# Performance work log

Hardware: AMD Instinct MI355X
Metric: run time of the kernel (lower is better)

Reference implementation:

```python
import jax, jax.numpy as jnp
import numpy as np

T, A, B_IMG, Z, READ_N, WRITE_N, ENC, DEC, BATCH = 16, 64, 64, 128, 8, 8, 512, 512, 512
EPS = 1e-8


def setup_inputs() -> dict:
    key = jax.random.key(0)
    ks = jax.random.split(key, 16)
    s = 0.05
    n = lambda k, shape: jax.random.normal(k, shape, jnp.float32) * s
    return {
        "x": jax.random.uniform(ks[0], (BATCH, B_IMG * A), jnp.float32),
        "eps": jax.random.normal(ks[1], (T, BATCH, Z), jnp.float32),
        "enc_Wih": n(ks[2], (4 * ENC, 2 * READ_N * READ_N + DEC)),
        "enc_Whh": n(ks[3], (4 * ENC, ENC)),
        "enc_b": jnp.zeros((4 * ENC,), jnp.float32),
        "mu_W": n(ks[4], (Z, ENC)),
        "mu_b": jnp.zeros((Z,), jnp.float32),
        "sig_W": n(ks[5], (Z, ENC)),
        "sig_b": jnp.zeros((Z,), jnp.float32),
        "dec_Wih": n(ks[6], (4 * DEC, Z)),
        "dec_Whh": n(ks[7], (4 * DEC, DEC)),
        "dec_b": jnp.zeros((4 * DEC,), jnp.float32),
        "write_W": n(ks[8], (WRITE_N * WRITE_N, DEC)),
        "write_b": jnp.zeros((WRITE_N * WRITE_N,), jnp.float32),
        "attn_W": n(ks[9], (5, DEC)),
        "attn_b": jnp.zeros((5,), jnp.float32),
    }


def _lstm(x, h, c, Wih, Whh, b):
    g = x @ Wih.T + h @ Whh.T + b  # [bs, 4H]
    i, f, gg, o = jnp.split(g, 4, axis=1)
    c2 = jax.nn.sigmoid(f) * c + jax.nn.sigmoid(i) * jnp.tanh(gg)
    return jax.nn.sigmoid(o) * jnp.tanh(c2), c2


def _filterbank(gx, gy, sigma2, delta, N):
    # gx, gy, sigma2, delta: [bs, 1]
    grid = jnp.arange(N, dtype=jnp.float32)[None, :]  # [1, N]
    mu_x = gx + (grid - 0.5 * N - 0.5) * delta  # [bs, N]
    mu_y = gy + (grid - 0.5 * N - 0.5) * delta
    a = jnp.arange(A, dtype=jnp.float32)
    b = jnp.arange(B_IMG, dtype=jnp.float32)
    s2 = sigma2[:, :, None]  # [bs,1,1]
    Fx = jnp.exp(-((a[None, None, :] - mu_x[:, :, None]) ** 2) / (2 * s2))  # [bs,N,A]
    Fx = Fx / (Fx.sum(2, keepdims=True) + EPS)
    Fy = jnp.exp(-((b[None, None, :] - mu_y[:, :, None]) ** 2) / (2 * s2))  # [bs,N,B]
    Fy = Fy / (Fy.sum(2, keepdims=True) + EPS)
    return Fx, Fy


def _attn_window(h_dec, N, attn_W, attn_b):
    p = h_dec @ attn_W.T + attn_b  # [bs,5]
    gx_, gy_, log_s2, log_d, log_g = jnp.split(p, 5, axis=1)
    gx = (A + 1) * 0.5 * (gx_ + 1)
    gy = (B_IMG + 1) * 0.5 * (gy_ + 1)
    delta = (max(A, B_IMG) - 1) * jnp.exp(log_d) / (N - 1)
    Fx, Fy = _filterbank(gx, gy, jnp.exp(log_s2), delta, N)
    return Fx, Fy, jnp.exp(log_g)  # gamma: [bs,1]


def reference(x, eps, enc_Wih, enc_Whh, enc_b, mu_W, mu_b, sig_W, sig_b,
              dec_Wih, dec_Whh, dec_b, write_W, write_b, attn_W, attn_b):
    bs = x.shape[0]
    img = x.reshape(bs, B_IMG, A)

    def step(carry, e):
        h_enc, c_enc, h_dec, c_dec, canvas = carry
        x_hat = x - jax.nn.sigmoid(canvas)
        # --- read with attention ---
        Fx, Fy, gamma = _attn_window(h_dec, READ_N, attn_W, attn_b)
        def glimpse(im):  # Fy @ im @ Fx^T -> [bs, N, N]
            g = jnp.einsum('bnh,bhw,bmw->bnm', Fy, im, Fx)
            return g.reshape(bs, READ_N * READ_N) * gamma
        r = jnp.concatenate([glimpse(img), glimpse(x_hat.reshape(bs, B_IMG, A))], axis=1)
        # --- encoder LSTM ---
        h_enc, c_enc = _lstm(jnp.concatenate([r, h_dec], 1), h_enc, c_enc, enc_Wih, enc_Whh, enc_b)
        # --- latent sample ---
        mu = h_enc @ mu_W.T + mu_b
        log_sigma = h_enc @ sig_W.T + sig_b
        z = mu + e * jnp.exp(log_sigma)
        # --- decoder LSTM ---
        h_dec, c_dec = _lstm(z, h_dec, c_dec, dec_Wih, dec_Whh, dec_b)
        # --- write with attention ---
        w = (h_dec @ write_W.T + write_b).reshape(bs, WRITE_N, WRITE_N)
        Fx2, Fy2, gamma2 = _attn_window(h_dec, WRITE_N, attn_W, attn_b)
        wr = jnp.einsum('bnh,bnm,bma->bha', Fy2, w, Fx2).reshape(bs, B_IMG * A) / gamma2
        canvas = canvas + wr
        return (h_enc, c_enc, h_dec, c_dec, canvas), canvas

    z32 = jnp.zeros((bs, ENC), jnp.float32)
    init = (z32, z32, jnp.zeros((bs, DEC), jnp.float32), jnp.zeros((bs, DEC), jnp.float32),
            jnp.zeros((bs, B_IMG * A), jnp.float32))
    _, cs = jax.lax.scan(step, init, eps)
    return cs  # [T, bs, B*A]
```

## Files before the change

### kernel.cpp

```cpp
#include <hip/hip_runtime.h>

#define LDF 68
#define EPSF 1e-8f
#define MFMA(A,B,C) __builtin_amdgcn_mfma_f32_16x16x32_bf16((A),(B),(C),0,0,0)

typedef __attribute__((ext_vector_type(8))) short bf16x8;
typedef __attribute__((ext_vector_type(4))) float f32x4;

__device__ __forceinline__ float sigf(float x){ return 1.0f/(1.0f + __expf(-x)); }

__device__ __forceinline__ unsigned short f2bf(float f){
  unsigned u = __float_as_uint(f);
  u += 0x7FFFu + ((u >> 16) & 1u);
  return (unsigned short)(u >> 16);
}
__device__ __forceinline__ float bf2f(unsigned short s){
  return __uint_as_float((unsigned)s << 16);
}

__device__ __forceinline__ size_t pk(int b, int col, int KB){
  return ((((size_t)((b>>4)*KB + (col>>5)))*64) + (size_t)((b&15) + (((col>>3)&3)<<4)))*8 + (col&7);
}

__device__ __forceinline__ void gload_lds16(const void* g, void* l){
  __builtin_amdgcn_global_load_lds(
      (const __attribute__((address_space(1))) void*)g,
      (__attribute__((address_space(3))) void*)l, 16, 0, 0);
}

__global__ void reorder_gates(const float* __restrict__ src, float* __restrict__ dst,
                              int H, int K, int total){
  int idx = blockIdx.x*256 + threadIdx.x;
  if (idx >= total) return;
  int row = idx / K;
  int col = idx - row*K;
  int j = row >> 2, g = row & 3;
  dst[idx] = src[(size_t)(g*H + j)*K + col];
}

__global__ void pack_w_mfma(const float* __restrict__ Wih, const float* __restrict__ Whh,
                            int K_ih, int K_tot,
                            unsigned short* __restrict__ dhi, unsigned short* __restrict__ dlo,
                            int total8){
  int idx = blockIdx.x*256 + threadIdx.x;
  if (idx >= total8) return;
  int lane = idx & 63;
  int rest = idx >> 6;
  int KB = K_tot >> 5;
  int kb = rest % KB;
  int fm = rest / KB;
  int rr = fm*16 + (lane & 15);
  int orow = (rr & 3)*512 + (rr >> 2);
  int k0 = kb*32 + (lane >> 4)*8;
  union { unsigned short s[8]; uint4 u; } vh, vl;
  #pragma unroll
  for (int i = 0; i < 8; i++){
    int k = k0 + i;
    float f = (k < K_ih) ? Wih[(size_t)orow*K_ih + k]
                         : Whh[(size_t)orow*512 + (k - K_ih)];
    unsigned short hi = f2bf(f);
    vh.s[i] = hi;
    vl.s[i] = f2bf(f - bf2f(hi));
  }
  *(uint4*)(dhi + (size_t)idx*8) = vh.u;
  *(uint4*)(dlo + (size_t)idx*8) = vl.u;
}

__global__ void pack_wz_mfma(const float* __restrict__ muW, const float* __restrict__ sigW,
                             unsigned short* __restrict__ dhi, unsigned short* __restrict__ dlo){
  int idx = blockIdx.x*256 + threadIdx.x;
  if (idx >= 16384) return;
  int lane = idx & 63, rest = idx >> 6;
  int kb = rest & 15, fmf = rest >> 4;
  int row = fmf*16 + (lane & 15);
  const float* src = (row < 128) ? (muW + (size_t)row*512) : (sigW + (size_t)(row-128)*512);
  int k0 = kb*32 + (lane >> 4)*8;
  union { unsigned short s[8]; uint4 u; } vh, vl;
  #pragma unroll
  for (int i = 0; i < 8; i++){
    float f = src[k0 + i];
    unsigned short hi = f2bf(f);
    vh.s[i] = hi;
    vl.s[i] = f2bf(f - bf2f(hi));
  }
  *(uint4*)(dhi + (size_t)idx*8) = vh.u;
  *(uint4*)(dlo + (size_t)idx*8) = vl.u;
}

__global__ void transpose_ww(const float* __restrict__ W, float* __restrict__ dst){
  int idx = blockIdx.x*256 + threadIdx.x;
  if (idx >= 512*64) return;
  int k = idx >> 6, n = idx & 63;
  dst[idx] = W[n*512 + k];
}

__global__ void zero_f(float* p, int n){
  int idx = blockIdx.x*256 + threadIdx.x;
  if (idx < n) p[idx] = 0.f;
}

__device__ void attn_window(const float* __restrict__ h,
                            const float* __restrict__ attn_W,
                            const float* __restrict__ attn_b,
                            float* Fx, float* Fy, float* pl)
{
  int tid = threadIdx.x;
  int lane = tid & 63, wid = tid >> 6;
  for (int q = wid; q < 5; q += 4){
    float s = 0.f;
    for (int k = lane; k < 512; k += 64) s += h[k]*attn_W[q*512 + k];
    for (int m = 32; m; m >>= 1) s += __shfl_xor(s, m);
    if (lane == 0) pl[q] = s + attn_b[q];
  }
  __syncthreads();
  float gx    = 32.5f*(pl[0] + 1.f);
  float gy    = 32.5f*(pl[1] + 1.f);
  float s2    = __expf(pl[2]);
  float delta = 9.f*__expf(pl[3]);
  float inv2  = 1.f/(2.f*s2);
  int n = tid >> 5, a = tid & 31;
  float mux = gx + ((float)n - 4.5f)*delta;
  float muy = gy + ((float)n - 4.5f)*delta;
  float dx0 = (float)a      - mux, dx1 = (float)(a+32) - mux;
  float dy0 = (float)a      - muy, dy1 = (float)(a+32) - muy;
  float e0 = __expf(-dx0*dx0*inv2), e1 = __expf(-dx1*dx1*inv2);
  float f0 = __expf(-dy0*dy0*inv2), f1 = __expf(-dy1*dy1*inv2);
  float sx = e0 + e1, sy = f0 + f1;
  for (int m = 16; m; m >>= 1){ sx += __shfl_xor(sx, m); sy += __shfl_xor(sy, m); }
  float rx = 1.f/(sx + EPSF), ry = 1.f/(sy + EPSF);
  Fx[n*LDF + a]      = e0*rx;  Fx[n*LDF + a + 32] = e1*rx;
  Fy[n*LDF + a]      = f0*ry;  Fy[n*LDF + a + 32] = f1*ry;
  __syncthreads();
}

template<int KB>
__global__ __launch_bounds__(512) void mfma_gemm_lstm(
    const bf16x8* __restrict__ Wh, const bf16x8* __restrict__ Wl,
    const unsigned short* __restrict__ act, int actPlane,
    const float4* __restrict__ bias4, const float* __restrict__ c_in,
    float* __restrict__ h_f32, float* __restrict__ c_out,
    unsigned short* __restrict__ out0, int KB0, int off0, int plane0,
    unsigned short* __restrict__ out1, int KB1, int off1, int plane1)
{
  __shared__ __align__(16) unsigned char lds[3][8192];
  const int tid = threadIdx.x, lane = tid & 63, w = tid >> 6;
  const int mt = blockIdx.x & 31, nt = blockIdx.x >> 5;
  const int fm = w & 3, fn0 = (w >> 2) << 1;

  const bf16x8* whp = Wh + ((size_t)(mt*4+fm)*KB)*64 + lane;
  const bf16x8* wlp = Wl + ((size_t)(mt*4+fm)*KB)*64 + lane;

  const char* ast = (const char*)act + (size_t)(w & 1)*((size_t)actPlane*2)
                  + ((size_t)(nt*4 + (w >> 1))*KB)*1024 + (size_t)lane*16;

  const int j0 = (mt*4+fm)*4 + (lane >> 4);
  float4 bb = bias4[j0];
  f32x4 acc0 = {bb.x, bb.y, bb.z, bb.w};
  f32x4 acc1 = acc0;

  gload_lds16(ast, (char*)&lds[0][w*1024]);
  bf16x8 whA = whp[0], wlA = wlp[0];
  __builtin_amdgcn_sched_barrier(0);
  asm volatile("" ::: "memory");
  gload_lds16(ast + 1024, (char*)&lds[1][w*1024]);
  bf16x8 whB = whp[64], wlB = wlp[64];
  __builtin_amdgcn_sched_barrier(0);
  asm volatile("" ::: "memory");

  const size_t rdoff = (size_t)fn0*2048 + (size_t)lane*16;

  #pragma unroll
  for (int kb = 0; kb < KB; kb++){
    asm volatile("s_waitcnt vmcnt(3)" ::: "memory");
    __builtin_amdgcn_s_barrier();
    asm volatile("" ::: "memory");
    __builtin_amdgcn_sched_barrier(0);
    bf16x8 whC = whA, wlC = wlA;
    if (kb + 2 < KB){
      gload_lds16(ast + (size_t)(kb+2)*1024, (char*)&lds[(kb+2)%3][w*1024]);
      whC = whp[(kb+2)*64]; wlC = wlp[(kb+2)*64];
    }
    const unsigned char* rb = &lds[kb%3][0] + rdoff;
    bf16x8 a0h = *(const bf16x8*)(rb);
    bf16x8 a0l = *(const bf16x8*)(rb + 1024);
    bf16x8 a1h = *(const bf16x8*)(rb + 2048);
    bf16x8 a1l = *(const bf16x8*)(rb + 3072);
    acc0 = MFMA(whA, a0h, acc0);
    acc1 = MFMA(whA, a1h, acc1);
    acc0 = MFMA(wlA, a0h, acc0);
    acc1 = MFMA(wlA, a1h, acc1);
    acc0 = MFMA(whA, a0l, acc0);
    acc1 = MFMA(whA, a1l, acc1);
    whA = whB; wlA = wlB; whB = whC; wlB = wlC;
  }

  const int bb0 = nt*64 + fn0*16 + (lane & 15);
  #pragma unroll
  for (int n = 0; n < 2; n++){
    f32x4 g = n ? acc1 : acc0;
    int b = bb0 + n*16;
    float ig = sigf(g[0]);
    float fg = sigf(g[1]);
    float gg = tanhf(g[2]);
    float og = sigf(g[3]);
    float c2 = fg * c_in[(size_t)b*512 + j0] + ig * gg;
    float h  = og * tanhf(c2);
    c_out[(size_t)b*512 + j0] = c2;
    if (h_f32) h_f32[(size_t)b*512 + j0] = h;
    unsigned short hh = f2bf(h);
    unsigned short hl = f2bf(h - bf2f(hh));
    size_t o0 = pk(b, off0 + j0, KB0);
    out0[o0] = hh; out0[o0 + plane0] = hl;
    if (out1){
      size_t o1 = pk(b, off1 + j0, KB1);
      out1[o1] = hh; out1[o1 + plane1] = hl;
    }
  }
}

__global__ __launch_bounds__(64) void zgemm_kernel(
    const bf16x8* __restrict__ Wzh, const bf16x8* __restrict__ Wzl,
    const unsigned short* __restrict__ az, int planeZ,
    const float* __restrict__ mu_b, const float* __restrict__ sig_b,
    const float* __restrict__ eps_t,
    unsigned short* __restrict__ actD, int planeD)
{
  const int fmb = blockIdx.x & 7, cg = blockIdx.x >> 3;
  const int lane = threadIdx.x;
  const bf16x8* wmh = Wzh + (size_t)(fmb    *16)*64 + lane;
  const bf16x8* wml = Wzl + (size_t)(fmb    *16)*64 + lane;
  const bf16x8* wsh = Wzh + (size_t)((fmb+8)*16)*64 + lane;
  const bf16x8* wsl = Wzl + (size_t)((fmb+8)*16)*64 + lane;
  const unsigned short* ab = az + (size_t)cg*8192 + (size_t)lane*8;

  const int r0 = fmb*16 + (lane >> 4)*4;
  float4 bm = *(const float4*)&mu_b[r0];
  float4 bs = *(const float4*)&sig_b[r0];
  f32x4 am = {bm.x, bm.y, bm.z, bm.w};
  f32x4 as = {bs.x, bs.y, bs.z, bs.w};

  #pragma unroll
  for (int kb = 0; kb < 16; kb++){
    bf16x8 ah = *(const bf16x8*)(ab + (size_t)kb*512);
    bf16x8 al = *(const bf16x8*)(ab + planeZ + (size_t)kb*512);
    bf16x8 h0 = wmh[kb*64], l0 = wml[kb*64];
    bf16x8 h1 = wsh[kb*64], l1 = wsl[kb*64];
    am = MFMA(h0, ah, am); am = MFMA(l0, ah, am); am = MFMA(h0, al, am);
    as = MFMA(h1, ah, as); as = MFMA(l1, ah, as); as = MFMA(h1, al, as);
  }

  const int b = cg*16 + (lane & 15);
  float4 ev = *(const float4*)&eps_t[(size_t)b*128 + r0];
  float e[4] = {ev.x, ev.y, ev.z, ev.w};
  union { unsigned short s[4]; uint2 u; } zh, zl;
  #pragma unroll
  for (int i = 0; i < 4; i++){
    float z = am[i] + e[i]*__expf(as[i]);
    unsigned short hi = f2bf(z);
    zh.s[i] = hi;
    zl.s[i] = f2bf(z - bf2f(hi));
  }
  size_t o = pk(b, r0, 20);
  *(uint2*)(actD + o) = zh.u;
  *(uint2*)(actD + planeD + o) = zl.u;
}

__global__ __launch_bounds__(256) void wg_kernel(
    const float* __restrict__ h_dec,
    const float* __restrict__ WwT, const float* __restrict__ write_b,
    const float* __restrict__ attn_W, const float* __restrict__ attn_b,
    const float* __restrict__ canvas_prev, float* __restrict__ canvas_out,
    const float* __restrict__ x,
    unsigned short* __restrict__ rout, int planeE)
{
  __shared__ float hs[512];
  __shared__ float Fx[8*LDF], Fy[8*LDF], pl[8];
  __shared__ float cs[64*LDF];
  __shared__ float img_s[64*LDF];
  __shared__ float P[2][8*LDF];
  __shared__ float ps[4][64], w_s[64];
  __shared__ float tmp[64*8];
  const int b = blockIdx.x, tid = threadIdx.x;

  for (int i = tid; i < 128; i += 256)
    ((float4*)hs)[i] = ((const float4*)(h_dec + (size_t)b*512))[i];
  if (rout){
    const float4* x4 = (const float4*)(x + (size_t)b*4096);
    for (int i = tid; i < 1024; i += 256){
      int row = i >> 4, cb = (i & 15)*4;
      *(float4*)&img_s[row*LDF + cb] = x4[i];
    }
  }
  __syncthreads();
  attn_window(hs, attn_W, attn_b, Fx, Fy, pl);
  float gamma = __expf(pl[4]);

  if (canvas_out){
    {
      int j = tid & 63, part = tid >> 6;
      float s = 0.f;
      int kb = part*128;
      for (int k = 0; k < 128; k++) s += hs[kb + k] * WwT[(kb + k)*64 + j];
      ps[part][j] = s;
    }
    __syncthreads();
    if (tid < 64)
      w_s[tid] = write_b[tid] + ps[0][tid] + ps[1][tid] + ps[2][tid] + ps[3][tid];
    __syncthreads();
    float inv_g = __expf(-pl[4]);
    #pragma unroll
    for (int e = 0; e < 2; e++){
      int gi = e*256 + tid;
      int m = gi & 7, hh = gi >> 3;
      float s = 0.f;
      #pragma unroll
      for (int nn = 0; nn < 8; nn++) s += Fy[nn*LDF + hh] * w_s[nn*8 + m];
      tmp[hh*8 + m] = s;
    }
    __syncthreads();
    for (int e = 0; e < 16; e++){
      int idx = e*256 + tid;
      int hh = idx >> 6, a = idx & 63;
      float s = 0.f;
      #pragma unroll
      for (int m = 0; m < 8; m++) s += tmp[hh*8 + m] * Fx[m*LDF + a];
      float prev = canvas_prev ? canvas_prev[(size_t)b*4096 + idx] : 0.f;
      float cv = prev + s*inv_g;
      canvas_out[(size_t)b*4096 + idx] = cv;
      cs[hh*LDF + a] = cv;
    }
  } else {
    for (int e = 0; e < 16; e++){
      int idx = e*256 + tid;
      cs[(idx >> 6)*LDF + (idx & 63)] = 0.f;
    }
  }
  if (!rout) return;
  __syncthreads();
  for (int e = 0; e < 16; e++){
    int idx = e*256 + tid;
    int hh = idx >> 6, a = idx & 63;
    cs[hh*LDF + a] = sigf(cs[hh*LDF + a]);
  }
  __syncthreads();
  #pragma unroll
  for (int e = 0; e < 4; e++){
    int gi = e*256 + tid;
    int d = gi >> 9, rem = gi & 511;
    int m = rem & 7, hh = rem >> 3;
    const float* S = d ? cs : img_s;
    float s = 0.f;
    #pragma unroll
    for (int w4 = 0; w4 < 64; w4 += 4){
      float4 iv = *(const float4*)&S[hh*LDF + w4];
      float4 fv = *(const float4*)&Fx[m*LDF + w4];
      s += iv.x*fv.x + iv.y*fv.y + iv.z*fv.z + iv.w*fv.w;
    }
    P[d][m*LDF + hh] = s;
  }
  __syncthreads();
  if (tid < 128){
    int d = tid >> 6, l = tid & 63;
    int n = l >> 3, m = l & 7;
    float s = 0.f;
    #pragma unroll
    for (int h4 = 0; h4 < 64; h4 += 4){
      float4 fv = *(const float4*)&Fy[n*LDF + h4];
      float4 pv = *(const float4*)&P[d][m*LDF + h4];
      s += fv.x*pv.x + fv.y*pv.y + fv.z*pv.z + fv.w*pv.w;
    }
    tmp[d*64 + l] = s;
  }
  __syncthreads();
  if (tid < 64){
    float g1 = tmp[tid]*gamma;
    float g2 = (tmp[tid] - tmp[64 + tid])*gamma;
    unsigned short h1 = f2bf(g1), l1 = f2bf(g1 - bf2f(h1));
    unsigned short h2 = f2bf(g2), l2 = f2bf(g2 - bf2f(h2));
    size_t o1 = pk(b, tid, 36);
    size_t o2 = pk(b, 64 + tid, 36);
    rout[o1] = h1; rout[o1 + planeE] = l1;
    rout[o2] = h2; rout[o2 + planeE] = l2;
  }
}

extern "C" void kernel_launch(void* const* d_in, const int* in_sizes, int n_in,
                              void* d_out, int out_size, void* d_ws, size_t ws_size,
                              hipStream_t stream)
{
  (void)in_sizes; (void)n_in; (void)out_size; (void)ws_size;
  const float* x       = (const float*)d_in[0];
  const float* eps     = (const float*)d_in[1];
  const float* encWih  = (const float*)d_in[2];
  const float* encWhh  = (const float*)d_in[3];
  const float* enc_b   = (const float*)d_in[4];
  const float* muW     = (const float*)d_in[5];
  const float* mu_b    = (const float*)d_in[6];
  const float* sigW    = (const float*)d_in[7];
  const float* sig_b   = (const float*)d_in[8];
  const float* decWih  = (const float*)d_in[9];
  const float* decWhh  = (const float*)d_in[10];
  const float* dec_b   = (const float*)d_in[11];
  const float* writeW  = (const float*)d_in[12];
  const float* write_b = (const float*)d_in[13];
  const float* attnW   = (const float*)d_in[14];
  const float* attn_b  = (const float*)d_in[15];
  float* out = (float*)d_out;

  char* p = (char*)d_ws;
  auto alloc = [&](size_t bytes){ char* r = p; p += (bytes + 255) & ~(size_t)255; return r; };

  const int KE = 1152, KD = 640;
  const int PE = 512*KE, PD = 512*KD, PZ = 512*512;
  const int T8E = 128*36*64, T8D = 128*20*64;

  unsigned short* WpEh = (unsigned short*)alloc((size_t)T8E*16);
  unsigned short* WpEl = (unsigned short*)alloc((size_t)T8E*16);
  unsigned short* WpDh = (unsigned short*)alloc((size_t)T8D*16);
  unsigned short* WpDl = (unsigned short*)alloc((size_t)T8D*16);
  unsigned short* Wzh  = (unsigned short*)alloc(16384*16);
  unsigned short* Wzl  = (unsigned short*)alloc(16384*16);
  float* bE  = (float*)alloc(2048*4);
  float* bD  = (float*)alloc(2048*4);
  float* WwT = (float*)alloc(512*64*4);
  char* z0 = p;
  unsigned short* actE0 = (unsigned short*)alloc((size_t)2*PE*2);
  unsigned short* actD0 = (unsigned short*)alloc((size_t)2*PD*2);
  float* hDf = (float*)alloc(512*512*4);
  float* cE0 = (float*)alloc(512*512*4);
  float* cD0 = (float*)alloc(512*512*4);
  size_t zbytes = (size_t)(p - z0);
  unsigned short* actE1 = (unsigned short*)alloc((size_t)2*PE*2);
  unsigned short* actD1 = (unsigned short*)alloc((size_t)2*PD*2);
  unsigned short* AZ    = (unsigned short*)alloc((size_t)2*PZ*2);
  float* cE1 = (float*)alloc(512*512*4);
  float* cD1 = (float*)alloc(512*512*4);

  unsigned short* actE[2] = { actE0, actE1 };
  unsigned short* actD[2] = { actD0, actD1 };
  float* cEf[2] = { cE0, cE1 };
  float* cDf[2] = { cD0, cD1 };

  int tot;
  tot = T8E;   pack_w_mfma<<<(tot+255)/256,256,0,stream>>>(encWih, encWhh, 640, KE, WpEh, WpEl, tot);
  tot = T8D;   pack_w_mfma<<<(tot+255)/256,256,0,stream>>>(decWih, decWhh, 128, KD, WpDh, WpDl, tot);
  pack_wz_mfma<<<64,256,0,stream>>>(muW, sigW, Wzh, Wzl);
  tot = 2048;  reorder_gates<<<(tot+255)/256,256,0,stream>>>(enc_b, bE, 512, 1, tot);
  tot = 2048;  reorder_gates<<<(tot+255)/256,256,0,stream>>>(dec_b, bD, 512, 1, tot);
  tot = 512*64; transpose_ww<<<(tot+255)/256,256,0,stream>>>(writeW, WwT);
  tot = (int)(zbytes/4); zero_f<<<(tot+255)/256,256,0,stream>>>((float*)z0, tot);

  wg_kernel<<<512,256,0,stream>>>(hDf, WwT, write_b, attnW, attn_b,
                                  nullptr, nullptr, x, actE[0], PE);

  for (int t = 0; t < 16; t++){
    int cur = t & 1, nxt = cur ^ 1;

    mfma_gemm_lstm<36><<<256,512,0,stream>>>(
        (const bf16x8*)WpEh, (const bf16x8*)WpEl, actE[cur], PE,
        (const float4*)bE, cEf[cur], nullptr, cEf[nxt],
        AZ, 16, 0, PZ,
        actE[nxt], 36, 640, PE);

    zgemm_kernel<<<256,64,0,stream>>>(
        (const bf16x8*)Wzh, (const bf16x8*)Wzl, AZ, PZ,
        mu_b, sig_b, eps + (size_t)t*65536, actD[cur], PD);

    mfma_gemm_lstm<20><<<256,512,0,stream>>>(
        (const bf16x8*)WpDh, (const bf16x8*)WpDl, actD[cur], PD,
        (const float4*)bD, cDf[cur], hDf, cDf[nxt],
        actE[nxt], 36, 128, PE,
        actD[nxt], 20, 128, PD);

    wg_kernel<<<512,256,0,stream>>>(hDf, WwT, write_b, attnW, attn_b,
                                    t ? (out + (size_t)(t-1)*2097152) : nullptr,
                                    out + (size_t)t*2097152, x,
                                    (t < 15) ? actE[nxt] : nullptr, PE);
  }
}
```

Baseline: 933.4 us.

## Retile LSTM GEMM to 8 M-fragments per block, split-K z-GEMM, fuse init kernels

The LSTM gate GEMM now gives each of the 8 waves its own weight M-fragment and has it cover all 4 batch N-fragments. This halves the grid to 128 blocks and lets each weight register load feed more activation reuse. The latent z GEMM moves from 64-thread blocks that loop over all 16 K-blocks to 512-thread blocks that split K across 8 waves and reduce the partials through shared memory, which shortens the serial MFMA chain. The small setup kernels are merged into a single launch. The trade-offs are fewer blocks on the GPU and more accumulator registers per wave.

```diff
diff --git a/kernel.cpp b/kernel.cpp
--- a/kernel.cpp
+++ b/kernel.cpp
@@ -26,16 +26,6 @@
   __builtin_amdgcn_global_load_lds(
       (const __attribute__((address_space(1))) void*)g,
       (__attribute__((address_space(3))) void*)l, 16, 0, 0);
-}
-
-__global__ void reorder_gates(const float* __restrict__ src, float* __restrict__ dst,
-                              int H, int K, int total){
-  int idx = blockIdx.x*256 + threadIdx.x;
-  if (idx >= total) return;
-  int row = idx / K;
-  int col = idx - row*K;
-  int j = row >> 2, g = row & 3;
-  dst[idx] = src[(size_t)(g*H + j)*K + col];
 }
 
 __global__ void pack_w_mfma(const float* __restrict__ Wih, const float* __restrict__ Whh,
@@ -66,37 +56,199 @@
   *(uint4*)(dlo + (size_t)idx*8) = vl.u;
 }
 
-__global__ void pack_wz_mfma(const float* __restrict__ muW, const float* __restrict__ sigW,
-                             unsigned short* __restrict__ dhi, unsigned short* __restrict__ dlo){
+__global__ void init_misc(const float* __restrict__ enc_b, const float* __restrict__ dec_b,
+                          const float* __restrict__ writeW,
+                          const float* __restrict__ muW, const float* __restrict__ sigW,
+                          float* __restrict__ bE, float* __restrict__ bD,
+                          float* __restrict__ WwT,
+                          unsigned short* __restrict__ Wzh, unsigned short* __restrict__ Wzl){
   int idx = blockIdx.x*256 + threadIdx.x;
-  if (idx >= 16384) return;
-  int lane = idx & 63, rest = idx >> 6;
-  int kb = rest & 15, fmf = rest >> 4;
-  int row = fmf*16 + (lane & 15);
-  const float* src = (row < 128) ? (muW + (size_t)row*512) : (sigW + (size_t)(row-128)*512);
-  int k0 = kb*32 + (lane >> 4)*8;
-  union { unsigned short s[8]; uint4 u; } vh, vl;
-  #pragma unroll
-  for (int i = 0; i < 8; i++){
-    float f = src[k0 + i];
-    unsigned short hi = f2bf(f);
-    vh.s[i] = hi;
-    vl.s[i] = f2bf(f - bf2f(hi));
-  }
-  *(uint4*)(dhi + (size_t)idx*8) = vh.u;
-  *(uint4*)(dlo + (size_t)idx*8) = vl.u;
-}
-
-__global__ void transpose_ww(const float* __restrict__ W, float* __restrict__ dst){
-  int idx = blockIdx.x*256 + threadIdx.x;
-  if (idx >= 512*64) return;
-  int k = idx >> 6, n = idx & 63;
-  dst[idx] = W[n*512 + k];
+  if (idx < 2048){
+    bE[idx] = enc_b[(idx & 3)*512 + (idx >> 2)];
+    return;
+  }
+  idx -= 2048;
+  if (idx < 2048){
+    bD[idx] = dec_b[(idx & 3)*512 + (idx >> 2)];
+    return;
+  }
+  idx -= 2048;
+  if (idx < 32768){
+    int k = idx >> 6, n = idx & 63;
+    WwT[idx] = writeW[n*512 + k];
+    return;
+  }
+  idx -= 32768;
+  if (idx < 16384){
+    int lane = idx & 63, rest = idx >> 6;
+    int kb = rest & 15, fmf = rest >> 4;
+    int row = fmf*16 + (lane & 15);
+    const float* src = (row < 128) ? (muW + (size_t)row*512) : (sigW + (size_t)(row-128)*512);
+    int k0 = kb*32 + (lane >> 4)*8;
+    union { unsigned short s[8]; uint4 u; } vh, vl;
+    #pragma unroll
+    for (int i = 0; i < 8; i++){
+      float f = src[k0 + i];
+      unsigned short hi = f2bf(f);
+      vh.s[i] = hi;
+      vl.s[i] = f2bf(f - bf2f(hi));
+    }
+    *(uint4*)(Wzh + (size_t)idx*8) = vh.u;
+    *(uint4*)(Wzl + (size_t)idx*8) = vl.u;
+  }
 }
 
 __global__ void zero_f(float* p, int n){
   int idx = blockIdx.x*256 + threadIdx.x;
   if (idx < n) p[idx] = 0.f;
+}
+
+template<int KB>
+__global__ __launch_bounds__(512) void mfma_gemm_lstm(
+    const bf16x8* __restrict__ Wh, const bf16x8* __restrict__ Wl,
+    const unsigned short* __restrict__ act, int actPlane,
+    const float4* __restrict__ bias4, const float* __restrict__ c_in,
+    float* __restrict__ h_f32, float* __restrict__ c_out,
+    unsigned short* __restrict__ out0, int KB0, int off0, int plane0,
+    unsigned short* __restrict__ out1, int KB1, int off1, int plane1)
+{
+  __shared__ __align__(16) unsigned char lds[3][8192];
+  const int tid = threadIdx.x, lane = tid & 63, w = tid >> 6;
+  const int mt = blockIdx.x & 15, nt = blockIdx.x >> 4;
+
+  const int fmg = mt*8 + w;
+  const bf16x8* whp = Wh + ((size_t)fmg*KB)*64 + lane;
+  const bf16x8* wlp = Wl + ((size_t)fmg*KB)*64 + lane;
+  const char* ast = (const char*)act + (size_t)(w & 1)*((size_t)actPlane*2)
+                  + ((size_t)(nt*4 + (w >> 1))*KB)*1024 + (size_t)lane*16;
+
+  const int j0 = fmg*4 + (lane >> 4);
+  float4 bb = bias4[j0];
+  f32x4 acc[4];
+  #pragma unroll
+  for (int fn = 0; fn < 4; fn++){ acc[fn][0]=bb.x; acc[fn][1]=bb.y; acc[fn][2]=bb.z; acc[fn][3]=bb.w; }
+
+  gload_lds16(ast, (char*)&lds[0][w*1024]);
+  bf16x8 whA = whp[0], wlA = wlp[0];
+  __builtin_amdgcn_sched_barrier(0);
+  asm volatile("" ::: "memory");
+  gload_lds16(ast + 1024, (char*)&lds[1][w*1024]);
+  bf16x8 whB = whp[64], wlB = wlp[64];
+  __builtin_amdgcn_sched_barrier(0);
+  asm volatile("" ::: "memory");
+
+  #pragma unroll
+  for (int kb = 0; kb < KB; kb++){
+    if (kb + 1 < KB) asm volatile("s_waitcnt vmcnt(3)" ::: "memory");
+    else             asm volatile("s_waitcnt vmcnt(0)" ::: "memory");
+    __builtin_amdgcn_s_barrier();
+    asm volatile("" ::: "memory");
+    __builtin_amdgcn_sched_barrier(0);
+    bf16x8 whC = whA, wlC = wlA;
+    if (kb + 2 < KB){
+      gload_lds16(ast + (size_t)(kb+2)*1024, (char*)&lds[(kb+2)%3][w*1024]);
+      whC = whp[(kb+2)*64]; wlC = wlp[(kb+2)*64];
+    }
+    const unsigned char* rb = &lds[kb%3][0] + (size_t)lane*16;
+    #pragma unroll
+    for (int fn = 0; fn < 4; fn++){
+      bf16x8 ah = *(const bf16x8*)(rb + fn*2048);
+      bf16x8 al = *(const bf16x8*)(rb + fn*2048 + 1024);
+      acc[fn] = MFMA(whA, ah, acc[fn]);
+      acc[fn] = MFMA(wlA, ah, acc[fn]);
+      acc[fn] = MFMA(whA, al, acc[fn]);
+    }
+    whA = whB; wlA = wlB; whB = whC; wlB = wlC;
+  }
+
+  const int bbase = nt*64 + (lane & 15);
+  #pragma unroll
+  for (int fn = 0; fn < 4; fn++){
+    f32x4 g = acc[fn];
+    int b = bbase + fn*16;
+    float ig = sigf(g[0]);
+    float fg = sigf(g[1]);
+    float gg = tanhf(g[2]);
+    float og = sigf(g[3]);
+    float c2 = fg * c_in[(size_t)b*512 + j0] + ig * gg;
+    float h  = og * tanhf(c2);
+    c_out[(size_t)b*512 + j0] = c2;
+    if (h_f32) h_f32[(size_t)b*512 + j0] = h;
+    unsigned short hh = f2bf(h);
+    unsigned short hl = f2bf(h - bf2f(hh));
+    size_t o0 = pk(b, off0 + j0, KB0);
+    out0[o0] = hh; out0[o0 + plane0] = hl;
+    if (out1){
+      size_t o1 = pk(b, off1 + j0, KB1);
+      out1[o1] = hh; out1[o1 + plane1] = hl;
+    }
+  }
+}
+
+__global__ __launch_bounds__(512) void zgemm8(
+    const unsigned short* __restrict__ Wzh, const unsigned short* __restrict__ Wzl,
+    const unsigned short* __restrict__ az, int planeZ,
+    const float* __restrict__ mu_b, const float* __restrict__ sig_b,
+    const float* __restrict__ eps_t,
+    unsigned short* __restrict__ actD, int planeD)
+{
+  __shared__ float zred[8*64*8];
+  const int tid = threadIdx.x, lane = tid & 63, w = tid >> 6;
+  const int fmb = blockIdx.x & 7, cg = blockIdx.x >> 3;
+  const char* azh = (const char*)az + (size_t)cg*16384 + (size_t)lane*16;
+  const char* azl = (const char*)(az + planeZ) + (size_t)cg*16384 + (size_t)lane*16;
+  const int kb0 = w*2;
+
+  bf16x8 a0h = *(const bf16x8*)(azh + (size_t)kb0*1024);
+  bf16x8 a0l = *(const bf16x8*)(azl + (size_t)kb0*1024);
+  bf16x8 a1h = *(const bf16x8*)(azh + (size_t)(kb0+1)*1024);
+  bf16x8 a1l = *(const bf16x8*)(azl + (size_t)(kb0+1)*1024);
+
+  const bf16x8* wmh = (const bf16x8*)Wzh + (size_t)(fmb    *16)*64 + lane;
+  const bf16x8* wml = (const bf16x8*)Wzl + (size_t)(fmb    *16)*64 + lane;
+  const bf16x8* wsh = (const bf16x8*)Wzh + (size_t)((fmb+8)*16)*64 + lane;
+  const bf16x8* wsl = (const bf16x8*)Wzl + (size_t)((fmb+8)*16)*64 + lane;
+  bf16x8 m0h = wmh[kb0*64],     m0l = wml[kb0*64];
+  bf16x8 s0h = wsh[kb0*64],     s0l = wsl[kb0*64];
+  bf16x8 m1h = wmh[(kb0+1)*64], m1l = wml[(kb0+1)*64];
+  bf16x8 s1h = wsh[(kb0+1)*64], s1l = wsl[(kb0+1)*64];
+
+  f32x4 am = {0.f,0.f,0.f,0.f}, as = {0.f,0.f,0.f,0.f};
+  am = MFMA(m0h,a0h,am); am = MFMA(m0l,a0h,am); am = MFMA(m0h,a0l,am);
+  as = MFMA(s0h,a0h,as); as = MFMA(s0l,a0h,as); as = MFMA(s0h,a0l,as);
+  am = MFMA(m1h,a1h,am); am = MFMA(m1l,a1h,am); am = MFMA(m1h,a1l,am);
+  as = MFMA(s1h,a1h,as); as = MFMA(s1l,a1h,as); as = MFMA(s1h,a1l,as);
+
+  *(f32x4*)&zred[(size_t)(w*64+lane)*8]     = am;
+  *(f32x4*)&zred[(size_t)(w*64+lane)*8 + 4] = as;
+  __syncthreads();
+
+  if (w == 0){
+    const int r0 = fmb*16 + (lane >> 4)*4;
+    float4 bm = *(const float4*)&mu_b[r0];
+    float4 bs = *(const float4*)&sig_b[r0];
+    f32x4 AM = {bm.x,bm.y,bm.z,bm.w};
+    f32x4 AS = {bs.x,bs.y,bs.z,bs.w};
+    #pragma unroll
+    for (int v = 0; v < 8; v++){
+      AM += *(f32x4*)&zred[(size_t)(v*64+lane)*8];
+      AS += *(f32x4*)&zred[(size_t)(v*64+lane)*8 + 4];
+    }
+    const int b = cg*16 + (lane & 15);
+    float4 ev = *(const float4*)&eps_t[(size_t)b*128 + r0];
+    float e[4] = {ev.x, ev.y, ev.z, ev.w};
+    union { unsigned short s[4]; uint2 u; } zh, zl;
+    #pragma unroll
+    for (int i = 0; i < 4; i++){
+      float z = AM[i] + e[i]*__expf(AS[i]);
+      unsigned short hi = f2bf(z);
+      zh.s[i] = hi;
+      zl.s[i] = f2bf(z - bf2f(hi));
+    }
+    size_t o = pk(b, r0, 20);
+    *(uint2*)(actD + o) = zh.u;
+    *(uint2*)(actD + planeD + o) = zl.u;
+  }
 }
 
 __device__ void attn_window(const float* __restrict__ h,
@@ -131,138 +283,6 @@
   Fx[n*LDF + a]      = e0*rx;  Fx[n*LDF + a + 32] = e1*rx;
   Fy[n*LDF + a]      = f0*ry;  Fy[n*LDF + a + 32] = f1*ry;
   __syncthreads();
-}
-
-template<int KB>
-__global__ __launch_bounds__(512) void mfma_gemm_lstm(
-    const bf16x8* __restrict__ Wh, const bf16x8* __restrict__ Wl,
-    const unsigned short* __restrict__ act, int actPlane,
-    const float4* __restrict__ bias4, const float* __restrict__ c_in,
-    float* __restrict__ h_f32, float* __restrict__ c_out,
-    unsigned short* __restrict__ out0, int KB0, int off0, int plane0,
-    unsigned short* __restrict__ out1, int KB1, int off1, int plane1)
-{
-  __shared__ __align__(16) unsigned char lds[3][8192];
-  const int tid = threadIdx.x, lane = tid & 63, w = tid >> 6;
-  const int mt = blockIdx.x & 31, nt = blockIdx.x >> 5;
-  const int fm = w & 3, fn0 = (w >> 2) << 1;
-
-  const bf16x8* whp = Wh + ((size_t)(mt*4+fm)*KB)*64 + lane;
-  const bf16x8* wlp = Wl + ((size_t)(mt*4+fm)*KB)*64 + lane;
-
-  const char* ast = (const char*)act + (size_t)(w & 1)*((size_t)actPlane*2)
-                  + ((size_t)(nt*4 + (w >> 1))*KB)*1024 + (size_t)lane*16;
-
-  const int j0 = (mt*4+fm)*4 + (lane >> 4);
-  float4 bb = bias4[j0];
-  f32x4 acc0 = {bb.x, bb.y, bb.z, bb.w};
-  f32x4 acc1 = acc0;
-
-  gload_lds16(ast, (char*)&lds[0][w*1024]);
-  bf16x8 whA = whp[0], wlA = wlp[0];
-  __builtin_amdgcn_sched_barrier(0);
-  asm volatile("" ::: "memory");
-  gload_lds16(ast + 1024, (char*)&lds[1][w*1024]);
-  bf16x8 whB = whp[64], wlB = wlp[64];
-  __builtin_amdgcn_sched_barrier(0);
-  asm volatile("" ::: "memory");
-
-  const size_t rdoff = (size_t)fn0*2048 + (size_t)lane*16;
-
-  #pragma unroll
-  for (int kb = 0; kb < KB; kb++){
-    asm volatile("s_waitcnt vmcnt(3)" ::: "memory");
-    __builtin_amdgcn_s_barrier();
-    asm volatile("" ::: "memory");
-    __builtin_amdgcn_sched_barrier(0);
-    bf16x8 whC = whA, wlC = wlA;
-    if (kb + 2 < KB){
-      gload_lds16(ast + (size_t)(kb+2)*1024, (char*)&lds[(kb+2)%3][w*1024]);
-      whC = whp[(kb+2)*64]; wlC = wlp[(kb+2)*64];
-    }
-    const unsigned char* rb = &lds[kb%3][0] + rdoff;
-    bf16x8 a0h = *(const bf16x8*)(rb);
-    bf16x8 a0l = *(const bf16x8*)(rb + 1024);
-    bf16x8 a1h = *(const bf16x8*)(rb + 2048);
-    bf16x8 a1l = *(const bf16x8*)(rb + 3072);
-    acc0 = MFMA(whA, a0h, acc0);
-    acc1 = MFMA(whA, a1h, acc1);
-    acc0 = MFMA(wlA, a0h, acc0);
-    acc1 = MFMA(wlA, a1h, acc1);
-    acc0 = MFMA(whA, a0l, acc0);
-    acc1 = MFMA(whA, a1l, acc1);
-    whA = whB; wlA = wlB; whB = whC; wlB = wlC;
-  }
-
-  const int bb0 = nt*64 + fn0*16 + (lane & 15);
-  #pragma unroll
-  for (int n = 0; n < 2; n++){
-    f32x4 g = n ? acc1 : acc0;
-    int b = bb0 + n*16;
-    float ig = sigf(g[0]);
-    float fg = sigf(g[1]);
-    float gg = tanhf(g[2]);
-    float og = sigf(g[3]);
-    float c2 = fg * c_in[(size_t)b*512 + j0] + ig * gg;
-    float h  = og * tanhf(c2);
-    c_out[(size_t)b*512 + j0] = c2;
-    if (h_f32) h_f32[(size_t)b*512 + j0] = h;
-    unsigned short hh = f2bf(h);
-    unsigned short hl = f2bf(h - bf2f(hh));
-    size_t o0 = pk(b, off0 + j0, KB0);
-    out0[o0] = hh; out0[o0 + plane0] = hl;
-    if (out1){
-      size_t o1 = pk(b, off1 + j0, KB1);
-      out1[o1] = hh; out1[o1 + plane1] = hl;
-    }
-  }
-}
-
-__global__ __launch_bounds__(64) void zgemm_kernel(
-    const bf16x8* __restrict__ Wzh, const bf16x8* __restrict__ Wzl,
-    const unsigned short* __restrict__ az, int planeZ,
-    const float* __restrict__ mu_b, const float* __restrict__ sig_b,
-    const float* __restrict__ eps_t,
-    unsigned short* __restrict__ actD, int planeD)
-{
-  const int fmb = blockIdx.x & 7, cg = blockIdx.x >> 3;
-  const int lane = threadIdx.x;
-  const bf16x8* wmh = Wzh + (size_t)(fmb    *16)*64 + lane;
-  const bf16x8* wml = Wzl + (size_t)(fmb    *16)*64 + lane;
-  const bf16x8* wsh = Wzh + (size_t)((fmb+8)*16)*64 + lane;
-  const bf16x8* wsl = Wzl + (size_t)((fmb+8)*16)*64 + lane;
-  const unsigned short* ab = az + (size_t)cg*8192 + (size_t)lane*8;
-
-  const int r0 = fmb*16 + (lane >> 4)*4;
-  float4 bm = *(const float4*)&mu_b[r0];
-  float4 bs = *(const float4*)&sig_b[r0];
-  f32x4 am = {bm.x, bm.y, bm.z, bm.w};
-  f32x4 as = {bs.x, bs.y, bs.z, bs.w};
-
-  #pragma unroll
-  for (int kb = 0; kb < 16; kb++){
-    bf16x8 ah = *(const bf16x8*)(ab + (size_t)kb*512);
-    bf16x8 al = *(const bf16x8*)(ab + planeZ + (size_t)kb*512);
-    bf16x8 h0 = wmh[kb*64], l0 = wml[kb*64];
-    bf16x8 h1 = wsh[kb*64], l1 = wsl[kb*64];
-    am = MFMA(h0, ah, am); am = MFMA(l0, ah, am); am = MFMA(h0, al, am);
-    as = MFMA(h1, ah, as); as = MFMA(l1, ah, as); as = MFMA(h1, al, as);
-  }
-
-  const int b = cg*16 + (lane & 15);
-  float4 ev = *(const float4*)&eps_t[(size_t)b*128 + r0];
-  float e[4] = {ev.x, ev.y, ev.z, ev.w};
-  union { unsigned short s[4]; uint2 u; } zh, zl;
-  #pragma unroll
-  for (int i = 0; i < 4; i++){
-    float z = am[i] + e[i]*__expf(as[i]);
-    unsigned short hi = f2bf(z);
-    zh.s[i] = hi;
-    zl.s[i] = f2bf(z - bf2f(hi));
-  }
-  size_t o = pk(b, r0, 20);
-  *(uint2*)(actD + o) = zh.u;
-  *(uint2*)(actD + planeD + o) = zl.u;
 }
 
 __global__ __launch_bounds__(256) void wg_kernel(
@@ -444,10 +464,9 @@
   int tot;
   tot = T8E;   pack_w_mfma<<<(tot+255)/256,256,0,stream>>>(encWih, encWhh, 640, KE, WpEh, WpEl, tot);
   tot = T8D;   pack_w_mfma<<<(tot+255)/256,256,0,stream>>>(decWih, decWhh, 128, KD, WpDh, WpDl, tot);
-  pack_wz_mfma<<<64,256,0,stream>>>(muW, sigW, Wzh, Wzl);
-  tot = 2048;  reorder_gates<<<(tot+255)/256,256,0,stream>>>(enc_b, bE, 512, 1, tot);
-  tot = 2048;  reorder_gates<<<(tot+255)/256,256,0,stream>>>(dec_b, bD, 512, 1, tot);
-  tot = 512*64; transpose_ww<<<(tot+255)/256,256,0,stream>>>(writeW, WwT);
+  tot = 2048+2048+32768+16384;
+  init_misc<<<(tot+255)/256,256,0,stream>>>(enc_b, dec_b, writeW, muW, sigW,
+                                            bE, bD, WwT, Wzh, Wzl);
   tot = (int)(zbytes/4); zero_f<<<(tot+255)/256,256,0,stream>>>((float*)z0, tot);
 
   wg_kernel<<<512,256,0,stream>>>(hDf, WwT, write_b, attnW, attn_b,
@@ -456,17 +475,17 @@
   for (int t = 0; t < 16; t++){
     int cur = t & 1, nxt = cur ^ 1;
 
-    mfma_gemm_lstm<36><<<256,512,0,stream>>>(
+    mfma_gemm_lstm<36><<<128,512,0,stream>>>(
         (const bf16x8*)WpEh, (const bf16x8*)WpEl, actE[cur], PE,
         (const float4*)bE, cEf[cur], nullptr, cEf[nxt],
         AZ, 16, 0, PZ,
         actE[nxt], 36, 640, PE);
 
-    zgemm_kernel<<<256,64,0,stream>>>(
-        (const bf16x8*)Wzh, (const bf16x8*)Wzl, AZ, PZ,
-        mu_b, sig_b, eps + (size_t)t*65536, actD[cur], PD);
-
-    mfma_gemm_lstm<20><<<256,512,0,stream>>>(
+    zgemm8<<<256,512,0,stream>>>(
+        Wzh, Wzl, AZ, PZ, mu_b, sig_b,
+        eps + (size_t)t*65536, actD[cur], PD);
+
+    mfma_gemm_lstm<20><<<128,512,0,stream>>>(
         (const bf16x8*)WpDh, (const bf16x8*)WpDl, actD[cur], PD,
         (const float4*)bD, cDf[cur], hDf, cDf[nxt],
         actE[nxt], 36, 128, PE,
```

After: 995.9 us. 1.07x slower.
